# Kernel tuning notes

Measured on AMD Instinct MI355X. Metric: run time of the kernel, lower is better.

Reference implementation:

```python
import jax, jax.numpy as jnp
import numpy as np

GROUP_SIZE = 256


def dequantize(qweight, scales, zeros, dtype):
    # qweight: [out, in] uint8-valued ints; scales/zeros: [n_groups, 1]
    out_f, in_f = qweight.shape
    w = qweight.astype(dtype).reshape(-1, GROUP_SIZE)
    w = (w - zeros) * scales
    return w.reshape(out_f, in_f)


def setup_inputs() -> dict:
    key = jax.random.key(0)
    k1, k2, k3, k4, k5 = jax.random.split(key, 5)
    B, S, IN, OUT = 4, 2048, 4096, 4096
    n_groups = OUT * IN // GROUP_SIZE
    x = jax.random.normal(k1, (B, S, IN), dtype=jnp.float32)
    qweight = jax.random.randint(k2, (OUT, IN), 0, 256, dtype=jnp.int32)
    scales = jax.random.uniform(k3, (n_groups, 1), dtype=jnp.float32) * 0.01 + 1e-4
    zeros = jax.random.randint(k4, (n_groups, 1), 0, 256).astype(jnp.float32)
    bias = jax.random.normal(k5, (OUT,), dtype=jnp.float32) * 0.02
    return {"x": x, "qweight": qweight, "scales": scales, "zeros": zeros, "bias": bias}


def reference(x, qweight, scales, zeros, bias):
    # float_weight = (qw - zeros) * scales, grouped along flattened weight
    w = dequantize(qweight, scales, zeros, x.dtype)  # [out, in]
    # y = x @ W^T + b
    return jnp.einsum("bsi,oi->bso", x, w) + bias
```

## Files before the change

### kernel.cpp

```cpp
#include <hip/hip_runtime.h>


typedef __attribute__((ext_vector_type(8))) short bf16x8;
typedef __attribute__((ext_vector_type(8))) unsigned short ushort8;
typedef __attribute__((ext_vector_type(4))) float f32x4;

__device__ inline unsigned short f2bf(float f) {
  union { float f; unsigned int u; } v; v.f = f;
  unsigned int u = v.u;
  return (unsigned short)((u + 0x7fffu + ((u >> 16) & 1u)) >> 16);
}

__global__ void dequant_w_kernel(const int* __restrict__ q,
                                 const float* __restrict__ sc,
                                 const float* __restrict__ zp,
                                 ushort8* __restrict__ wb, int total8) {
  int t = blockIdx.x * blockDim.x + threadIdx.x;
  if (t >= total8) return;
  const int4* q4 = (const int4*)q + (size_t)t * 2;
  int4 a = q4[0];
  int4 b = q4[1];
  int g = t >> 5;
  float s = sc[g], z = zp[g];
  ushort8 o;
  o[0] = f2bf(((float)a.x - z) * s);
  o[1] = f2bf(((float)a.y - z) * s);
  o[2] = f2bf(((float)a.z - z) * s);
  o[3] = f2bf(((float)a.w - z) * s);
  o[4] = f2bf(((float)b.x - z) * s);
  o[5] = f2bf(((float)b.y - z) * s);
  o[6] = f2bf(((float)b.z - z) * s);
  o[7] = f2bf(((float)b.w - z) * s);
  wb[t] = o;
}

__global__ void convert_x_kernel(const float* __restrict__ x,
                                 ushort8* __restrict__ xb, int total8) {
  int t = blockIdx.x * blockDim.x + threadIdx.x;
  if (t >= total8) return;
  const float4* x4 = (const float4*)x + (size_t)t * 2;
  float4 a = x4[0];
  float4 b = x4[1];
  ushort8 o;
  o[0] = f2bf(a.x); o[1] = f2bf(a.y); o[2] = f2bf(a.z); o[3] = f2bf(a.w);
  o[4] = f2bf(b.x); o[5] = f2bf(b.y); o[6] = f2bf(b.z); o[7] = f2bf(b.w);
  xb[t] = o;
}

#define BM 256
#define BN 256
#define BK 64

#define BAR()       asm volatile("s_barrier" ::: "memory")
#define WAIT_LGKM0() asm volatile("s_waitcnt lgkmcnt(0)" ::: "memory")
#define MFMA_(d, x, y) d = __builtin_amdgcn_mfma_f32_16x16x32_bf16(x, y, d, 0, 0, 0)

__device__ inline void gload_lds16(const void* g, void* l) {
  __builtin_amdgcn_global_load_lds(
      (const __attribute__((address_space(1))) unsigned int*)g,
      (__attribute__((address_space(3))) unsigned int*)l, 16, 0, 0);
}

__device__ inline void stage_half(const unsigned short* __restrict__ gsrc,
                                  char* lds_region, int K, int wave, int lane) {
  const int l3  = lane >> 3;
  const int swz = ((lane & 7) ^ l3) * 8;
#pragma unroll
  for (int inst = 0; inst < 2; ++inst) {
    const int row = inst * 64 + wave * 8 + l3;
    gload_lds16(gsrc + (size_t)row * K + swz,
                lds_region + (size_t)(inst * 512 + wave * 64) * 16);
  }
}

__global__ __launch_bounds__(512, 2)
void gemm256_kernel(const unsigned short* __restrict__ A,
                    const unsigned short* __restrict__ B,
                    const float* __restrict__ bias,
                    float* __restrict__ C,
                    int M, int N, int K) {
  extern __shared__ char lds[];
  const int t    = threadIdx.x;
  const int lane = t & 63;
  const int wave = t >> 6;
  const int wm   = wave >> 2;
  const int wn   = wave & 3;
  const int lr   = lane & 15;
  const int hi   = lane >> 4;
  const int l7   = lane & 7;

  const int nwg = gridDim.x;
  const int cpx = nwg >> 3;
  const int bid = blockIdx.x;
  const int swzb = (bid & 7) * cpx + (bid >> 3);
  const int ntn = N / BN;
  const int bm = swzb / ntn, bn = swzb % ntn;
  const int row0 = bm * BM, col0 = bn * BN;

  const int NT = K / BK;

  const int soff0 = (((0) + hi) ^ l7) * 16;
  const int soff1 = (((4) + hi) ^ l7) * 16;

  const unsigned short* Asrc = A + (size_t)row0 * K;
  const unsigned short* Bsrc = B + (size_t)col0 * K;

#define STAGE_B0(buf, kt) stage_half(Bsrc + (size_t)(kt) * BK,               (buf) + 32768,         K, wave, lane)
#define STAGE_B1(buf, kt) stage_half(Bsrc + (size_t)128 * K + (kt) * BK,     (buf) + 32768 + 16384, K, wave, lane)
#define STAGE_A0(buf, kt) stage_half(Asrc + (size_t)(kt) * BK,               (buf),                 K, wave, lane)
#define STAGE_A1(buf, kt) stage_half(Asrc + (size_t)128 * K + (kt) * BK,     (buf) + 16384,         K, wave, lane)

  f32x4 acc[8][4] = {};
  bf16x8 a[4][2], b[4][2];

  char* buf0 = lds;
  char* buf1 = lds + 65536;
  STAGE_B0(buf0, 0); STAGE_B1(buf0, 0); STAGE_A0(buf0, 0); STAGE_A1(buf0, 0);
  asm volatile("s_waitcnt vmcnt(4)" ::: "memory");
  STAGE_B0(buf1, 1); STAGE_B1(buf1, 1); STAGE_A0(buf1, 1);
  asm volatile("s_waitcnt vmcnt(6)" ::: "memory");
  BAR();

  for (int kt = 0; kt < NT; ++kt) {
    char* buf  = lds + ((size_t)(kt & 1) << 16);
    char* nbuf = lds + ((size_t)((kt & 1) ^ 1) << 16);
    const char* Ab = buf;
    const char* Bb = buf + 32768;

#pragma unroll
    for (int mm = 0; mm < 4; ++mm) {
      const int r = (wm * 128 + mm * 16 + lr) * 128;
      a[mm][0] = *(const bf16x8*)(Ab + r + soff0);
      a[mm][1] = *(const bf16x8*)(Ab + r + soff1);
    }
#pragma unroll
    for (int n = 0; n < 2; ++n) {
      const int r = (wn * 64 + n * 16 + lr) * 128;
      b[n][0] = *(const bf16x8*)(Bb + r + soff0);
      b[n][1] = *(const bf16x8*)(Bb + r + soff1);
    }
    if (kt + 1 < NT) STAGE_A1(nbuf, kt + 1);
    asm volatile("s_waitcnt lgkmcnt(8)" ::: "memory");
    BAR();
    WAIT_LGKM0();
    __builtin_amdgcn_s_setprio(1);
#pragma unroll
    for (int mm = 0; mm < 4; ++mm)
#pragma unroll
      for (int n = 0; n < 2; ++n) {
        MFMA_(acc[mm][n], a[mm][0], b[n][0]);
        MFMA_(acc[mm][n], a[mm][1], b[n][1]);
      }
    __builtin_amdgcn_s_setprio(0);
    BAR();

#pragma unroll
    for (int n = 2; n < 4; ++n) {
      const int r = (wn * 64 + n * 16 + lr) * 128;
      b[n][0] = *(const bf16x8*)(Bb + r + soff0);
      b[n][1] = *(const bf16x8*)(Bb + r + soff1);
    }
    if (kt + 2 < NT) STAGE_B0(buf, kt + 2);
    BAR();
    WAIT_LGKM0();
    __builtin_amdgcn_s_setprio(1);
#pragma unroll
    for (int mm = 0; mm < 4; ++mm)
#pragma unroll
      for (int n = 2; n < 4; ++n) {
        MFMA_(acc[mm][n], a[mm][0], b[n][0]);
        MFMA_(acc[mm][n], a[mm][1], b[n][1]);
      }
    __builtin_amdgcn_s_setprio(0);
    BAR();

#pragma unroll
    for (int mm = 0; mm < 4; ++mm) {
      const int r = (wm * 128 + 64 + mm * 16 + lr) * 128;
      a[mm][0] = *(const bf16x8*)(Ab + r + soff0);
      a[mm][1] = *(const bf16x8*)(Ab + r + soff1);
    }
    if (kt + 2 < NT) STAGE_B1(buf, kt + 2);
    BAR();
    WAIT_LGKM0();
    __builtin_amdgcn_s_setprio(1);
#pragma unroll
    for (int mm = 0; mm < 4; ++mm)
#pragma unroll
      for (int n = 0; n < 2; ++n) {
        MFMA_(acc[4 + mm][n], a[mm][0], b[n][0]);
        MFMA_(acc[4 + mm][n], a[mm][1], b[n][1]);
      }
    __builtin_amdgcn_s_setprio(0);
    BAR();

    if (kt + 2 < NT) STAGE_A0(buf, kt + 2);
    BAR();
    __builtin_amdgcn_s_setprio(1);
#pragma unroll
    for (int mm = 0; mm < 4; ++mm)
#pragma unroll
      for (int n = 2; n < 4; ++n) {
        MFMA_(acc[4 + mm][n], a[mm][0], b[n][0]);
        MFMA_(acc[4 + mm][n], a[mm][1], b[n][1]);
      }
    __builtin_amdgcn_s_setprio(0);
    if (kt < NT - 2)      asm volatile("s_waitcnt vmcnt(6)" ::: "memory");
    else if (kt == NT - 2) asm volatile("s_waitcnt vmcnt(0)" ::: "memory");
    BAR();
  }

#pragma unroll
  for (int n = 0; n < 4; ++n) {
    const int col = col0 + wn * 64 + n * 16 + lr;
    const float bv = bias[col];
#pragma unroll
    for (int m = 0; m < 8; ++m) {
      const int rbase = row0 + wm * 128 + m * 16 + hi * 4;
#pragma unroll
      for (int j = 0; j < 4; ++j)
        C[(size_t)(rbase + j) * N + col] = acc[m][n][j] + bv;
    }
  }
#undef STAGE_B0
#undef STAGE_B1
#undef STAGE_A0
#undef STAGE_A1
}

extern "C" void kernel_launch(void* const* d_in, const int* in_sizes, int n_in,
                              void* d_out, int out_size, void* d_ws, size_t ws_size,
                              hipStream_t stream) {
  const float* x      = (const float*)d_in[0];
  const int*   qw     = (const int*)d_in[1];
  const float* scales = (const float*)d_in[2];
  const float* zeros  = (const float*)d_in[3];
  const float* bias   = (const float*)d_in[4];
  float* out = (float*)d_out;

  const int OUT = in_sizes[4];
  const int IN  = in_sizes[1] / OUT;
  const int M   = in_sizes[0] / IN;

  unsigned short* wb = (unsigned short*)d_ws;
  unsigned short* xb = wb + (size_t)OUT * IN;

  {
    int total8 = OUT * IN / 8;
    dequant_w_kernel<<<(total8 + 255) / 256, 256, 0, stream>>>(
        qw, scales, zeros, (ushort8*)wb, total8);
  }
  {
    int total8 = (int)((size_t)M * IN / 8);
    convert_x_kernel<<<(total8 + 255) / 256, 256, 0, stream>>>(
        x, (ushort8*)xb, total8);
  }
  {
    hipFuncSetAttribute((const void*)gemm256_kernel,
                        hipFuncAttributeMaxDynamicSharedMemorySize, 131072);
    dim3 grid((M / BM) * (OUT / BN));
    gemm256_kernel<<<grid, 512, 131072, stream>>>(xb, wb, bias, out, M, OUT, IN);
  }
}
```

Baseline: 293.2 us.

## Switch GEMM inner loop to 32x32x16 bf16 MFMA with restructured LDS fragment loads

Replaces the 16x16x32 MFMA tiling with 32x32x16 MFMAs, so each wave computes 4x2 tiles of 32x32 with 16-wide accumulators. LDS fragment loads and the swizzle offsets are reworked to match the new operand layout, and the staging schedule is rearranged (B1 and A0 are now issued together, and one early vmcnt wait is dropped). The larger MFMA raises the arithmetic per LDS read and cuts instruction count, at the cost of changed register pressure and a different pipeline interleave whose wait counts must still match.

```diff
diff --git a/kernel.cpp b/kernel.cpp
--- a/kernel.cpp
+++ b/kernel.cpp
@@ -1,9 +1,9 @@
 #include <hip/hip_runtime.h>
 
 
-typedef __attribute__((ext_vector_type(8))) short bf16x8;
-typedef __attribute__((ext_vector_type(8))) unsigned short ushort8;
-typedef __attribute__((ext_vector_type(4))) float f32x4;
+typedef __attribute__((ext_vector_type(8)))  short bf16x8;
+typedef __attribute__((ext_vector_type(8)))  unsigned short ushort8;
+typedef __attribute__((ext_vector_type(16))) float f32x16;
 
 __device__ inline unsigned short f2bf(float f) {
   union { float f; unsigned int u; } v; v.f = f;
@@ -51,9 +51,9 @@
 #define BN 256
 #define BK 64
 
-#define BAR()       asm volatile("s_barrier" ::: "memory")
+#define BAR()        asm volatile("s_barrier" ::: "memory")
 #define WAIT_LGKM0() asm volatile("s_waitcnt lgkmcnt(0)" ::: "memory")
-#define MFMA_(d, x, y) d = __builtin_amdgcn_mfma_f32_16x16x32_bf16(x, y, d, 0, 0, 0)
+#define MFMA32(d, x, y) d = __builtin_amdgcn_mfma_f32_32x32x16_bf16(x, y, d, 0, 0, 0)
 
 __device__ inline void gload_lds16(const void* g, void* l) {
   __builtin_amdgcn_global_load_lds(
@@ -85,9 +85,9 @@
   const int wave = t >> 6;
   const int wm   = wave >> 2;
   const int wn   = wave & 3;
-  const int lr   = lane & 15;
-  const int hi   = lane >> 4;
-  const int l7   = lane & 7;
+  const int l31  = lane & 31;
+  const int hi32 = lane >> 5;
+  const int sx   = lane & 7;
 
   const int nwg = gridDim.x;
   const int cpx = nwg >> 3;
@@ -99,24 +99,31 @@
 
   const int NT = K / BK;
 
-  const int soff0 = (((0) + hi) ^ l7) * 16;
-  const int soff1 = (((4) + hi) ^ l7) * 16;
-
   const unsigned short* Asrc = A + (size_t)row0 * K;
   const unsigned short* Bsrc = B + (size_t)col0 * K;
 
-#define STAGE_B0(buf, kt) stage_half(Bsrc + (size_t)(kt) * BK,               (buf) + 32768,         K, wave, lane)
-#define STAGE_B1(buf, kt) stage_half(Bsrc + (size_t)128 * K + (kt) * BK,     (buf) + 32768 + 16384, K, wave, lane)
-#define STAGE_A0(buf, kt) stage_half(Asrc + (size_t)(kt) * BK,               (buf),                 K, wave, lane)
-#define STAGE_A1(buf, kt) stage_half(Asrc + (size_t)128 * K + (kt) * BK,     (buf) + 16384,         K, wave, lane)
-
-  f32x4 acc[8][4] = {};
-  bf16x8 a[4][2], b[4][2];
+#define STAGE_B0(buf, kt) stage_half(Bsrc + (size_t)(kt) * BK,           (buf) + 32768, K, wave, lane)
+#define STAGE_B1(buf, kt) stage_half(Bsrc + (size_t)128 * K + (kt) * BK, (buf) + 49152, K, wave, lane)
+#define STAGE_A0(buf, kt) stage_half(Asrc + (size_t)(kt) * BK,           (buf),         K, wave, lane)
+#define STAGE_A1(buf, kt) stage_half(Asrc + (size_t)128 * K + (kt) * BK, (buf) + 16384, K, wave, lane)
+
+  const int aReg = wm * 16384;
+  const int bReg = 32768 + (wn >> 1) * 16384;
+  const int aRow0 = (0 * 32 + l31) * 128;
+  const int aRow1 = (1 * 32 + l31) * 128;
+  const int aRow2 = (2 * 32 + l31) * 128;
+  const int aRow3 = (3 * 32 + l31) * 128;
+  const int bRow0 = ((wn & 1) * 64 + 0 * 32 + l31) * 128;
+  const int bRow1 = ((wn & 1) * 64 + 1 * 32 + l31) * 128;
+#define SOFF(ks) ((((ks) * 2 + hi32) ^ sx) * 16)
+
+  f32x16 acc[4][2] = {};
+  bf16x8 a[2][4];
+  bf16x8 b[2][4];
 
   char* buf0 = lds;
   char* buf1 = lds + 65536;
   STAGE_B0(buf0, 0); STAGE_B1(buf0, 0); STAGE_A0(buf0, 0); STAGE_A1(buf0, 0);
-  asm volatile("s_waitcnt vmcnt(4)" ::: "memory");
   STAGE_B0(buf1, 1); STAGE_B1(buf1, 1); STAGE_A0(buf1, 1);
   asm volatile("s_waitcnt vmcnt(6)" ::: "memory");
   BAR();
@@ -124,20 +131,14 @@
   for (int kt = 0; kt < NT; ++kt) {
     char* buf  = lds + ((size_t)(kt & 1) << 16);
     char* nbuf = lds + ((size_t)((kt & 1) ^ 1) << 16);
-    const char* Ab = buf;
-    const char* Bb = buf + 32768;
-
-#pragma unroll
-    for (int mm = 0; mm < 4; ++mm) {
-      const int r = (wm * 128 + mm * 16 + lr) * 128;
-      a[mm][0] = *(const bf16x8*)(Ab + r + soff0);
-      a[mm][1] = *(const bf16x8*)(Ab + r + soff1);
-    }
-#pragma unroll
-    for (int n = 0; n < 2; ++n) {
-      const int r = (wn * 64 + n * 16 + lr) * 128;
-      b[n][0] = *(const bf16x8*)(Bb + r + soff0);
-      b[n][1] = *(const bf16x8*)(Bb + r + soff1);
+    const char* Ab = buf + aReg;
+    const char* Bb = buf + bReg;
+
+#pragma unroll
+    for (int ks = 0; ks < 4; ++ks) {
+      a[0][ks] = *(const bf16x8*)(Ab + aRow0 + SOFF(ks));
+      a[1][ks] = *(const bf16x8*)(Ab + aRow1 + SOFF(ks));
+      b[0][ks] = *(const bf16x8*)(Bb + bRow0 + SOFF(ks));
     }
     if (kt + 1 < NT) STAGE_A1(nbuf, kt + 1);
     asm volatile("s_waitcnt lgkmcnt(8)" ::: "memory");
@@ -145,87 +146,77 @@
     WAIT_LGKM0();
     __builtin_amdgcn_s_setprio(1);
 #pragma unroll
-    for (int mm = 0; mm < 4; ++mm)
-#pragma unroll
-      for (int n = 0; n < 2; ++n) {
-        MFMA_(acc[mm][n], a[mm][0], b[n][0]);
-        MFMA_(acc[mm][n], a[mm][1], b[n][1]);
-      }
-    __builtin_amdgcn_s_setprio(0);
-    BAR();
-
-#pragma unroll
-    for (int n = 2; n < 4; ++n) {
-      const int r = (wn * 64 + n * 16 + lr) * 128;
-      b[n][0] = *(const bf16x8*)(Bb + r + soff0);
-      b[n][1] = *(const bf16x8*)(Bb + r + soff1);
+    for (int ks = 0; ks < 4; ++ks) {
+      MFMA32(acc[0][0], a[0][ks], b[0][ks]);
+      MFMA32(acc[1][0], a[1][ks], b[0][ks]);
+    }
+    __builtin_amdgcn_s_setprio(0);
+    BAR();
+
+#pragma unroll
+    for (int ks = 0; ks < 4; ++ks)
+      b[1][ks] = *(const bf16x8*)(Bb + bRow1 + SOFF(ks));
+    BAR();
+    WAIT_LGKM0();
+    __builtin_amdgcn_s_setprio(1);
+#pragma unroll
+    for (int ks = 0; ks < 4; ++ks) {
+      MFMA32(acc[0][1], a[0][ks], b[1][ks]);
+      MFMA32(acc[1][1], a[1][ks], b[1][ks]);
+    }
+    __builtin_amdgcn_s_setprio(0);
+    BAR();
+
+#pragma unroll
+    for (int ks = 0; ks < 4; ++ks) {
+      a[0][ks] = *(const bf16x8*)(Ab + aRow2 + SOFF(ks));
+      a[1][ks] = *(const bf16x8*)(Ab + aRow3 + SOFF(ks));
     }
     if (kt + 2 < NT) STAGE_B0(buf, kt + 2);
     BAR();
     WAIT_LGKM0();
     __builtin_amdgcn_s_setprio(1);
 #pragma unroll
-    for (int mm = 0; mm < 4; ++mm)
-#pragma unroll
-      for (int n = 2; n < 4; ++n) {
-        MFMA_(acc[mm][n], a[mm][0], b[n][0]);
-        MFMA_(acc[mm][n], a[mm][1], b[n][1]);
-      }
-    __builtin_amdgcn_s_setprio(0);
-    BAR();
-
-#pragma unroll
-    for (int mm = 0; mm < 4; ++mm) {
-      const int r = (wm * 128 + 64 + mm * 16 + lr) * 128;
-      a[mm][0] = *(const bf16x8*)(Ab + r + soff0);
-      a[mm][1] = *(const bf16x8*)(Ab + r + soff1);
-    }
-    if (kt + 2 < NT) STAGE_B1(buf, kt + 2);
-    BAR();
-    WAIT_LGKM0();
-    __builtin_amdgcn_s_setprio(1);
-#pragma unroll
-    for (int mm = 0; mm < 4; ++mm)
-#pragma unroll
-      for (int n = 0; n < 2; ++n) {
-        MFMA_(acc[4 + mm][n], a[mm][0], b[n][0]);
-        MFMA_(acc[4 + mm][n], a[mm][1], b[n][1]);
-      }
-    __builtin_amdgcn_s_setprio(0);
-    BAR();
-
-    if (kt + 2 < NT) STAGE_A0(buf, kt + 2);
-    BAR();
-    __builtin_amdgcn_s_setprio(1);
-#pragma unroll
-    for (int mm = 0; mm < 4; ++mm)
-#pragma unroll
-      for (int n = 2; n < 4; ++n) {
-        MFMA_(acc[4 + mm][n], a[mm][0], b[n][0]);
-        MFMA_(acc[4 + mm][n], a[mm][1], b[n][1]);
-      }
-    __builtin_amdgcn_s_setprio(0);
-    if (kt < NT - 2)      asm volatile("s_waitcnt vmcnt(6)" ::: "memory");
-    else if (kt == NT - 2) asm volatile("s_waitcnt vmcnt(0)" ::: "memory");
-    BAR();
-  }
-
-#pragma unroll
-  for (int n = 0; n < 4; ++n) {
-    const int col = col0 + wn * 64 + n * 16 + lr;
+    for (int ks = 0; ks < 4; ++ks) {
+      MFMA32(acc[2][0], a[0][ks], b[0][ks]);
+      MFMA32(acc[3][0], a[1][ks], b[0][ks]);
+    }
+    __builtin_amdgcn_s_setprio(0);
+    BAR();
+
+    if (kt + 2 < NT) { STAGE_B1(buf, kt + 2); STAGE_A0(buf, kt + 2); }
+    BAR();
+    __builtin_amdgcn_s_setprio(1);
+#pragma unroll
+    for (int ks = 0; ks < 4; ++ks) {
+      MFMA32(acc[2][1], a[0][ks], b[1][ks]);
+      MFMA32(acc[3][1], a[1][ks], b[1][ks]);
+    }
+    __builtin_amdgcn_s_setprio(0);
+    if (kt + 2 < NT)      asm volatile("s_waitcnt vmcnt(6)" ::: "memory");
+    else if (kt + 1 < NT) asm volatile("s_waitcnt vmcnt(0)" ::: "memory");
+    BAR();
+  }
+
+#pragma unroll
+  for (int g = 0; g < 2; ++g) {
+    const int col = col0 + wn * 64 + g * 32 + l31;
     const float bv = bias[col];
 #pragma unroll
-    for (int m = 0; m < 8; ++m) {
-      const int rbase = row0 + wm * 128 + m * 16 + hi * 4;
-#pragma unroll
-      for (int j = 0; j < 4; ++j)
-        C[(size_t)(rbase + j) * N + col] = acc[m][n][j] + bv;
+    for (int f = 0; f < 4; ++f) {
+      const int rbase = row0 + wm * 128 + f * 32 + 4 * hi32;
+#pragma unroll
+      for (int q = 0; q < 4; ++q)
+#pragma unroll
+        for (int j = 0; j < 4; ++j)
+          C[(size_t)(rbase + 8 * q + j) * N + col] = acc[f][g][q * 4 + j] + bv;
     }
   }
 #undef STAGE_B0
 #undef STAGE_B1
 #undef STAGE_A0
 #undef STAGE_A1
+#undef SOFF
 }
 
 extern "C" void kernel_launch(void* const* d_in, const int* in_sizes, int n_in,
```

New measurement: 318.7 us. +8.7%, slower.

## Software-pipeline LDS fragment reads behind MFMAs and halve barriers in the GEMM loop

Applied to the files above, without the earlier changes.

Restructures the bf16 GEMM main loop so each quadrant's LDS fragment reads are issued right after the previous quadrant's MFMAs. The first A/B fragments of the next k-tile are prefetched at the end of the current iteration. This drops the explicit lgkmcnt waits and cuts the barriers per k-tile from eight to four, so LDS latency and global-to-LDS staging overlap more with matrix math. The trade-off is that the overlap now depends on compiler-inserted waits and reordered vmcnt accounting, which adds register pressure and risks subtle LDS read/write hazards.

```diff
diff --git a/kernel.cpp b/kernel.cpp
--- a/kernel.cpp
+++ b/kernel.cpp
@@ -51,9 +51,8 @@
 #define BN 256
 #define BK 64
 
-#define BAR()       asm volatile("s_barrier" ::: "memory")
-#define WAIT_LGKM0() asm volatile("s_waitcnt lgkmcnt(0)" ::: "memory")
-#define MFMA_(d, x, y) d = __builtin_amdgcn_mfma_f32_16x16x32_bf16(x, y, d, 0, 0, 0)
+#define BAR() asm volatile("s_barrier" ::: "memory")
+#define MFMA16(d, x, y) d = __builtin_amdgcn_mfma_f32_16x16x32_bf16(x, y, d, 0, 0, 0)
 
 __device__ inline void gload_lds16(const void* g, void* l) {
   __builtin_amdgcn_global_load_lds(
@@ -99,115 +98,87 @@
 
   const int NT = K / BK;
 
-  const int soff0 = (((0) + hi) ^ l7) * 16;
-  const int soff1 = (((4) + hi) ^ l7) * 16;
+  const int soff0 = ((hi) ^ l7) * 16;
+  const int soff1 = ((4 + hi) ^ l7) * 16;
 
   const unsigned short* Asrc = A + (size_t)row0 * K;
   const unsigned short* Bsrc = B + (size_t)col0 * K;
 
-#define STAGE_B0(buf, kt) stage_half(Bsrc + (size_t)(kt) * BK,               (buf) + 32768,         K, wave, lane)
-#define STAGE_B1(buf, kt) stage_half(Bsrc + (size_t)128 * K + (kt) * BK,     (buf) + 32768 + 16384, K, wave, lane)
-#define STAGE_A0(buf, kt) stage_half(Asrc + (size_t)(kt) * BK,               (buf),                 K, wave, lane)
-#define STAGE_A1(buf, kt) stage_half(Asrc + (size_t)128 * K + (kt) * BK,     (buf) + 16384,         K, wave, lane)
+#define STAGE_A0(buf, kt) stage_half(Asrc + (size_t)(kt) * BK,           (buf),         K, wave, lane)
+#define STAGE_A1(buf, kt) stage_half(Asrc + (size_t)128 * K + (kt) * BK, (buf) + 16384, K, wave, lane)
+#define STAGE_B0(buf, kt) stage_half(Bsrc + (size_t)(kt) * BK,           (buf) + 32768, K, wave, lane)
+#define STAGE_B1(buf, kt) stage_half(Bsrc + (size_t)128 * K + (kt) * BK, (buf) + 49152, K, wave, lane)
 
   f32x4 acc[8][4] = {};
-  bf16x8 a[4][2], b[4][2];
+  bf16x8 a[4][2];
+  bf16x8 b[4][2];
+
+#define READ_A(mh, bufp) {                                                    \
+    const char* Ab_ = (const char*)(bufp) + wm * 16384 + (mh) * 8192;         \
+    _Pragma("unroll")                                                         \
+    for (int mm = 0; mm < 4; ++mm) {                                          \
+      const int r_ = (mm * 16 + lr) * 128;                                    \
+      a[mm][0] = *(const bf16x8*)(Ab_ + r_ + soff0);                          \
+      a[mm][1] = *(const bf16x8*)(Ab_ + r_ + soff1);                          \
+    } }
+#define READ_B(nh, bufp) {                                                    \
+    const char* Bb_ = (const char*)(bufp) + 32768 + wn * 8192;                \
+    _Pragma("unroll")                                                         \
+    for (int nn = 0; nn < 2; ++nn) {                                          \
+      const int r_ = (((nh) * 2 + nn) * 16 + lr) * 128;                       \
+      b[(nh) * 2 + nn][0] = *(const bf16x8*)(Bb_ + r_ + soff0);               \
+      b[(nh) * 2 + nn][1] = *(const bf16x8*)(Bb_ + r_ + soff1);               \
+    } }
+#define MFMA_QUAD(mh, nh)                                                     \
+    __builtin_amdgcn_s_setprio(1);                                            \
+    _Pragma("unroll")                                                         \
+    for (int mm = 0; mm < 4; ++mm)                                            \
+      _Pragma("unroll")                                                       \
+      for (int nn = 0; nn < 2; ++nn) {                                        \
+        MFMA16(acc[(mh) * 4 + mm][(nh) * 2 + nn], a[mm][0], b[(nh) * 2 + nn][0]); \
+        MFMA16(acc[(mh) * 4 + mm][(nh) * 2 + nn], a[mm][1], b[(nh) * 2 + nn][1]); \
+      }                                                                       \
+    __builtin_amdgcn_s_setprio(0);
 
   char* buf0 = lds;
   char* buf1 = lds + 65536;
-  STAGE_B0(buf0, 0); STAGE_B1(buf0, 0); STAGE_A0(buf0, 0); STAGE_A1(buf0, 0);
-  asm volatile("s_waitcnt vmcnt(4)" ::: "memory");
-  STAGE_B0(buf1, 1); STAGE_B1(buf1, 1); STAGE_A0(buf1, 1);
+  STAGE_A0(buf0, 0); STAGE_A1(buf0, 0); STAGE_B0(buf0, 0); STAGE_B1(buf0, 0);
+  STAGE_A0(buf1, 1); STAGE_B0(buf1, 1); STAGE_B1(buf1, 1);
   asm volatile("s_waitcnt vmcnt(6)" ::: "memory");
   BAR();
+  READ_A(0, buf0);
+  READ_B(0, buf0);
 
   for (int kt = 0; kt < NT; ++kt) {
     char* buf  = lds + ((size_t)(kt & 1) << 16);
     char* nbuf = lds + ((size_t)((kt & 1) ^ 1) << 16);
-    const char* Ab = buf;
-    const char* Bb = buf + 32768;
-
-#pragma unroll
-    for (int mm = 0; mm < 4; ++mm) {
-      const int r = (wm * 128 + mm * 16 + lr) * 128;
-      a[mm][0] = *(const bf16x8*)(Ab + r + soff0);
-      a[mm][1] = *(const bf16x8*)(Ab + r + soff1);
+
+    BAR();
+    MFMA_QUAD(0, 0);
+    if (kt + 1 < NT) STAGE_A1(nbuf, kt + 1);
+    READ_B(1, buf);
+
+    BAR();
+    MFMA_QUAD(0, 1);
+    if (kt + 2 < NT) STAGE_B0(buf, kt + 2);
+    READ_A(1, buf);
+
+    BAR();
+    MFMA_QUAD(1, 0);
+    if (kt + 2 < NT) {
+      STAGE_B1(buf, kt + 2);
+      asm volatile("s_waitcnt vmcnt(4)" ::: "memory");
+    } else {
+      asm volatile("s_waitcnt vmcnt(0)" ::: "memory");
     }
-#pragma unroll
-    for (int n = 0; n < 2; ++n) {
-      const int r = (wn * 64 + n * 16 + lr) * 128;
-      b[n][0] = *(const bf16x8*)(Bb + r + soff0);
-      b[n][1] = *(const bf16x8*)(Bb + r + soff1);
+
+    BAR();
+    MFMA_QUAD(1, 1);
+    if (kt + 2 < NT) STAGE_A0(buf, kt + 2);
+    if (kt + 1 < NT) {
+      READ_A(0, nbuf);
+      READ_B(0, nbuf);
     }
-    if (kt + 1 < NT) STAGE_A1(nbuf, kt + 1);
-    asm volatile("s_waitcnt lgkmcnt(8)" ::: "memory");
-    BAR();
-    WAIT_LGKM0();
-    __builtin_amdgcn_s_setprio(1);
-#pragma unroll
-    for (int mm = 0; mm < 4; ++mm)
-#pragma unroll
-      for (int n = 0; n < 2; ++n) {
-        MFMA_(acc[mm][n], a[mm][0], b[n][0]);
-        MFMA_(acc[mm][n], a[mm][1], b[n][1]);
-      }
-    __builtin_amdgcn_s_setprio(0);
-    BAR();
-
-#pragma unroll
-    for (int n = 2; n < 4; ++n) {
-      const int r = (wn * 64 + n * 16 + lr) * 128;
-      b[n][0] = *(const bf16x8*)(Bb + r + soff0);
-      b[n][1] = *(const bf16x8*)(Bb + r + soff1);
-    }
-    if (kt + 2 < NT) STAGE_B0(buf, kt + 2);
-    BAR();
-    WAIT_LGKM0();
-    __builtin_amdgcn_s_setprio(1);
-#pragma unroll
-    for (int mm = 0; mm < 4; ++mm)
-#pragma unroll
-      for (int n = 2; n < 4; ++n) {
-        MFMA_(acc[mm][n], a[mm][0], b[n][0]);
-        MFMA_(acc[mm][n], a[mm][1], b[n][1]);
-      }
-    __builtin_amdgcn_s_setprio(0);
-    BAR();
-
-#pragma unroll
-    for (int mm = 0; mm < 4; ++mm) {
-      const int r = (wm * 128 + 64 + mm * 16 + lr) * 128;
-      a[mm][0] = *(const bf16x8*)(Ab + r + soff0);
-      a[mm][1] = *(const bf16x8*)(Ab + r + soff1);
-    }
-    if (kt + 2 < NT) STAGE_B1(buf, kt + 2);
-    BAR();
-    WAIT_LGKM0();
-    __builtin_amdgcn_s_setprio(1);
-#pragma unroll
-    for (int mm = 0; mm < 4; ++mm)
-#pragma unroll
-      for (int n = 0; n < 2; ++n) {
-        MFMA_(acc[4 + mm][n], a[mm][0], b[n][0]);
-        MFMA_(acc[4 + mm][n], a[mm][1], b[n][1]);
-      }
-    __builtin_amdgcn_s_setprio(0);
-    BAR();
-
-    if (kt + 2 < NT) STAGE_A0(buf, kt + 2);
-    BAR();
-    __builtin_amdgcn_s_setprio(1);
-#pragma unroll
-    for (int mm = 0; mm < 4; ++mm)
-#pragma unroll
-      for (int n = 2; n < 4; ++n) {
-        MFMA_(acc[4 + mm][n], a[mm][0], b[n][0]);
-        MFMA_(acc[4 + mm][n], a[mm][1], b[n][1]);
-      }
-    __builtin_amdgcn_s_setprio(0);
-    if (kt < NT - 2)      asm volatile("s_waitcnt vmcnt(6)" ::: "memory");
-    else if (kt == NT - 2) asm volatile("s_waitcnt vmcnt(0)" ::: "memory");
-    BAR();
   }
 
 #pragma unroll
@@ -222,10 +193,13 @@
         C[(size_t)(rbase + j) * N + col] = acc[m][n][j] + bv;
     }
   }
+#undef STAGE_A0
+#undef STAGE_A1
 #undef STAGE_B0
 #undef STAGE_B1
-#undef STAGE_A0
-#undef STAGE_A1
+#undef READ_A
+#undef READ_B
+#undef MFMA_QUAD
 }
 
 extern "C" void kernel_launch(void* const* d_in, const int* in_sizes, int n_in,
```

After: 279.0 us. -4.8%, faster.
